# Optimization experiments

Hardware: AMD Instinct MI355X
Metric: run time of the kernel (lower is better)

## Reference

```python
import jax, jax.numpy as jnp
import numpy as np

DIM = 1024
NUM_HEADS = 1  # module's proj-after-squeeze only type-checks with 1 head
HEAD_DIM = DIM // NUM_HEADS
NQ = 8192
NK = 8192
B = 1


def setup_inputs() -> dict:
    key = jax.random.key(0)
    ks = jax.random.split(key, 12)
    s = 0.02  # weight init scale
    return {
        "q": jax.random.normal(ks[0], (NQ, B, DIM), jnp.float32),
        "k": jax.random.normal(ks[1], (NK, B, DIM), jnp.float32),
        "v": jax.random.normal(ks[2], (NK, B, DIM), jnp.float32),
        "ref_boxes": jax.random.uniform(ks[3], (NK, B, 4), jnp.float32),
        "query_boxes": jax.random.uniform(ks[4], (NQ, B, 4), jnp.float32),
        "Wq": jax.random.normal(ks[5], (DIM, DIM), jnp.float32) * s,
        "Wk": jax.random.normal(ks[6], (DIM, DIM), jnp.float32) * s,
        "Wv": jax.random.normal(ks[7], (DIM, DIM), jnp.float32) * s,
        "Wp": jax.random.normal(ks[8], (DIM, DIM), jnp.float32) * s,
        "bp": jnp.zeros((DIM,), jnp.float32),
        "W1": jax.random.normal(ks[9], (DIM, 2 * DIM), jnp.float32) * s,
        "b1": jnp.zeros((2 * DIM,), jnp.float32),
        "W2": jax.random.normal(ks[10], (2 * DIM, NUM_HEADS), jnp.float32) * s,
        "b2": jnp.zeros((NUM_HEADS,), jnp.float32),
    }


def _centers(boxes):  # [N, B, 4] -> [B, N, 2]
    c = (boxes[..., :2] + boxes[..., 2:]) * 0.5
    return jnp.transpose(c, (1, 0, 2))


def reference(q, k, v, ref_boxes, query_boxes, Wq, Wk, Wv, Wp, bp, W1, b1, W2, b2):
    Nq, Bsz, dim = q.shape
    Nk = k.shape[0]
    H = W2.shape[1]
    hd = dim // H
    scale = hd ** -0.5

    # bias_weight = sigmoid(MLP(var(k, dim=0)))  -- torch.var is unbiased (ddof=1)
    gfv = jnp.var(k, axis=0, ddof=1)                       # [B, dim]
    bias_weight = jax.nn.sigmoid(
        jax.nn.relu(gfv @ W1 + b1) @ W2 + b2
    )                                                       # [B, H]

    # seq-first -> batch-first, project, split heads
    qb = jnp.transpose(q, (1, 0, 2))                        # [B, Nq, dim]
    kb = jnp.transpose(k, (1, 0, 2))
    vb = jnp.transpose(v, (1, 0, 2))
    qh = (qb @ Wq).reshape(Bsz, Nq, H, hd).transpose(0, 2, 1, 3) * scale
    kh = (kb @ Wk).reshape(Bsz, Nk, H, hd).transpose(0, 2, 1, 3)
    vh = (vb @ Wv).reshape(Bsz, Nk, H, hd).transpose(0, 2, 1, 3)

    attn = jnp.einsum('bhqd,bhkd->bhqk', qh, kh)            # [B, H, Nq, Nk]

    # relative-position bias: per-head learned weight * (-pairwise box-center distance)
    cq = _centers(query_boxes)                              # [B, Nq, 2]
    cr = _centers(ref_boxes)                                # [B, Nk, 2]
    d2 = jnp.sum((cq[:, :, None, :] - cr[:, None, :, :]) ** 2, axis=-1)
    dist = jnp.sqrt(d2 + 1e-8)                              # [B, Nq, Nk]
    attn = attn - bias_weight[:, :, None, None] * dist[:, None, :, :]

    attn = jax.nn.softmax(attn, axis=-1)
    x = jnp.einsum('bhqk,bhkd->bhqd', attn, vh)             # [B, H, Nq, hd]
    x = jnp.squeeze(x)                                      # [Nq, dim] since B=H=1
    return x @ Wp + bp
```

## Files before the change

kernel.cpp:

```cpp
#include <hip/hip_runtime.h>
#include <math.h>

#define DIM 1024
#define NQ 8192
#define NK 8192

typedef unsigned short u16;
typedef __attribute__((ext_vector_type(8))) short short8;
typedef __attribute__((ext_vector_type(8))) u16 u16x8;
typedef __attribute__((ext_vector_type(4))) u16 u16x4;
typedef __attribute__((ext_vector_type(4))) float f32x4;
typedef __attribute__((address_space(1))) const unsigned int gu32;
typedef __attribute__((address_space(3))) unsigned int lu32;

__device__ inline u16 f2bf(float f) {
  unsigned u = __builtin_bit_cast(unsigned, f);
  u += 0x7fff + ((u >> 16) & 1);
  return (u16)(u >> 16);
}
__device__ inline float bf2f(u16 h) {
  unsigned u = ((unsigned)h) << 16;
  return __builtin_bit_cast(float, u);
}


__global__ void var_partial_kernel(const float* __restrict__ k,
                                   float* __restrict__ ps, float* __restrict__ pq) {
  int col = blockIdx.x * 256 + threadIdx.x;
  int r0  = blockIdx.y * 256;
  float s = 0.f, q = 0.f;
  for (int r = 0; r < 256; ++r) {
    float x = k[(size_t)(r0 + r) * DIM + col];
    s += x; q += x * x;
  }
  ps[blockIdx.y * DIM + col] = s;
  pq[blockIdx.y * DIM + col] = q;
}

__global__ void gfv_kernel(const float* __restrict__ ps, const float* __restrict__ pq,
                           float* __restrict__ gfv) {
  int col = blockIdx.x * 256 + threadIdx.x;
  float s = 0.f, q = 0.f;
  for (int c = 0; c < 32; ++c) { s += ps[c * DIM + col]; q += pq[c * DIM + col]; }
  const float n = 8192.f;
  gfv[col] = (q - s * s / n) / (n - 1.f);
}

__global__ void h1_partial_kernel(const float* __restrict__ gfv, const float* __restrict__ W1,
                                  float* __restrict__ h1p) {
  int j  = blockIdx.x * 256 + threadIdx.x;
  int d0 = blockIdx.y * 128;
  float acc = 0.f;
  for (int d = 0; d < 128; ++d)
    acc += gfv[d0 + d] * W1[(size_t)(d0 + d) * 2048 + j];
  h1p[blockIdx.y * 2048 + j] = acc;
}

__global__ void bw_kernel(const float* __restrict__ h1p, const float* __restrict__ b1,
                          const float* __restrict__ W2, const float* __restrict__ b2,
                          float* __restrict__ bw) {
  __shared__ float red[256];
  int t = threadIdx.x;
  float acc = 0.f;
  for (int i = 0; i < 8; ++i) {
    int j = i * 256 + t;
    float h = b1[j];
    for (int c = 0; c < 8; ++c) h += h1p[c * 2048 + j];
    h = fmaxf(h, 0.f);
    acc += h * W2[j];
  }
  red[t] = acc; __syncthreads();
  for (int s = 128; s > 0; s >>= 1) { if (t < s) red[t] += red[t + s]; __syncthreads(); }
  if (t == 0) bw[0] = 1.f / (1.f + __expf(-(red[0] + b2[0])));
}

__global__ void centers_kernel(const float4* __restrict__ qb, const float4* __restrict__ rb,
                               const float* __restrict__ bwp,
                               float2* __restrict__ cq, float2* __restrict__ cr,
                               float2* __restrict__ cqs, float2* __restrict__ crs) {
  int i = blockIdx.x * 256 + threadIdx.x;
  const float sc = bwp[0] * 1.44269504f;
  float4 a = qb[i];
  float2 c1 = make_float2(0.5f * (a.x + a.z), 0.5f * (a.y + a.w));
  cq[i] = c1;
  cqs[i] = make_float2(c1.x * sc, c1.y * sc);
  float4 b = rb[i];
  float2 c2 = make_float2(0.5f * (b.x + b.z), 0.5f * (b.y + b.w));
  cr[i] = c2;
  crs[i] = make_float2(c2.x * sc, c2.y * sc);
}


__global__ void f2bf3_kernel(const float4* __restrict__ a, const float4* __restrict__ b,
                             const float4* __restrict__ c, u16x4* __restrict__ oa,
                             u16x4* __restrict__ ob, u16x4* __restrict__ oc, int n4) {
  const float4* in = (blockIdx.y == 0) ? a : (blockIdx.y == 1) ? b : c;
  u16x4* out = (blockIdx.y == 0) ? oa : (blockIdx.y == 1) ? ob : oc;
  for (int i = blockIdx.x * 256 + threadIdx.x; i < n4; i += gridDim.x * 256) {
    float4 v = in[i];
    u16x4 o;
    o[0] = f2bf(v.x); o[1] = f2bf(v.y); o[2] = f2bf(v.z); o[3] = f2bf(v.w);
    out[i] = o;
  }
}

__global__ __launch_bounds__(256) void wtrans4_kernel(
    const float* __restrict__ W0, const float* __restrict__ W1,
    const float* __restrict__ W2, const float* __restrict__ W3,
    u16* __restrict__ T0, u16* __restrict__ T1, u16* __restrict__ T2, u16* __restrict__ T3) {
  const float* W = (blockIdx.z == 0) ? W0 : (blockIdx.z == 1) ? W1 : (blockIdx.z == 2) ? W2 : W3;
  u16* WT = (blockIdx.z == 0) ? T0 : (blockIdx.z == 1) ? T1 : (blockIdx.z == 2) ? T2 : T3;
  __shared__ float tile[64][65];
  const int t = threadIdx.x;
  const int kb = blockIdx.x * 64, nb = blockIdx.y * 64;
#pragma unroll
  for (int i = 0; i < 16; ++i) {
    int r = i * 4 + (t >> 6), c = t & 63;
    tile[c][r] = W[(size_t)(kb + r) * 1024 + nb + c];
  }
  __syncthreads();
#pragma unroll
  for (int i = 0; i < 16; ++i) {
    int n = i * 4 + (t >> 6), kk = t & 63;
    WT[(size_t)(nb + n) * 1024 + kb + kk] = f2bf(tile[n][kk]);
  }
}


#define TM 128
#define TN 128
#define TK 32

template <int OUT>
__global__ __launch_bounds__(256) void bgemm_kernel(
    const u16* __restrict__ A, const u16* __restrict__ Bt, void* __restrict__ C,
    const float* __restrict__ bias, int M, int N, int K, int ldc, float alpha) {
  __shared__ __align__(16) u16 As[TM * TK];
  __shared__ __align__(16) u16 Bs[TN * TK];

  const int t = threadIdx.x;
  const int l = t & 63;
  const int w = t >> 6;
  const int wm = w >> 1, wn = w & 1;
  const size_t row0 = (size_t)blockIdx.y * TM;
  const size_t col0 = (size_t)blockIdx.x * TN;

  f32x4 acc[4][4];
#pragma unroll
  for (int m = 0; m < 4; ++m)
#pragma unroll
    for (int n = 0; n < 4; ++n) acc[m][n] = (f32x4){0.f, 0.f, 0.f, 0.f};

  const int lane_r = l & 15;
  const int kgrp = (l >> 4) * 8;

  for (int k0 = 0; k0 < K; k0 += TK) {
#pragma unroll
    for (int j = 0; j < 2; ++j) {
      int idx = j * 256 + t;
      int r = idx >> 2, c8 = (idx & 3) << 3;
      __builtin_amdgcn_global_load_lds((gu32*)(A + (row0 + r) * K + k0 + c8),
                                       (lu32*)(As + idx * 8), 16, 0, 0);
      __builtin_amdgcn_global_load_lds((gu32*)(Bt + (col0 + r) * K + k0 + c8),
                                       (lu32*)(Bs + idx * 8), 16, 0, 0);
    }
    __syncthreads();

    short8 a[4], b[4];
#pragma unroll
    for (int m = 0; m < 4; ++m)
      a[m] = *(const short8*)&As[(wm * 64 + m * 16 + lane_r) * TK + kgrp];
#pragma unroll
    for (int n = 0; n < 4; ++n)
      b[n] = *(const short8*)&Bs[(wn * 64 + n * 16 + lane_r) * TK + kgrp];
#pragma unroll
    for (int m = 0; m < 4; ++m)
#pragma unroll
      for (int n = 0; n < 4; ++n)
        acc[m][n] = __builtin_amdgcn_mfma_f32_16x16x32_bf16(a[m], b[n], acc[m][n], 0, 0, 0);
    __syncthreads();
  }

#pragma unroll
  for (int m = 0; m < 4; ++m) {
#pragma unroll
    for (int n = 0; n < 4; ++n) {
      size_t col = col0 + wn * 64 + n * 16 + lane_r;
      size_t rbase = row0 + wm * 64 + m * 16 + (l >> 4) * 4;
      if (OUT == 0) {
        float bv = bias[col];
#pragma unroll
        for (int j = 0; j < 4; ++j)
          ((float*)C)[(rbase + j) * (size_t)ldc + col] = acc[m][n][j] * alpha + bv;
      } else if (OUT == 1) {
#pragma unroll
        for (int j = 0; j < 4; ++j)
          ((u16*)C)[(rbase + j) * (size_t)ldc + col] = f2bf(acc[m][n][j] * alpha);
      } else {
        u16x4 p;
#pragma unroll
        for (int j = 0; j < 4; ++j) p[j] = f2bf(acc[m][n][j] * alpha);
        *(u16x4*)&((u16*)C)[col * (size_t)ldc + rbase] = p;
      }
    }
  }
}


template <int VM>
__device__ __forceinline__ void waitvm() {
  if constexpr (VM == 4) asm volatile("s_waitcnt vmcnt(4)" ::: "memory");
  else asm volatile("s_waitcnt vmcnt(0)" ::: "memory");
}
#define FENCE asm volatile("" ::: "memory")
#define BARRIER do { FENCE; __builtin_amdgcn_s_barrier(); FENCE; } while (0)

#define SGA(UNIT, KT, BUF)                                                          \
  __builtin_amdgcn_global_load_lds(                                                 \
      (gu32*)(Agp + (size_t)((UNIT) * 64) * ldaB + (size_t)(KT) * 128),             \
      (lu32*)(smem + (BUF) * 16384 + (UNIT) * 4096 + tid * 8), 16, 0, 0)

#define SGB(UNIT, KT, BUF)                                                          \
  do {                                                                              \
    int _rp = (UNIT) * 64 + rr;                                                     \
    size_t _row = (size_t)(bn0 + ((_rp >> 5) & 3) * 64 + (_rp >> 7) * 32 + (_rp & 31)); \
    __builtin_amdgcn_global_load_lds(                                               \
        (gu32*)(Bgp + _row * ldbB + (size_t)(KT) * 128),                            \
        (lu32*)(smem + 32768 + (BUF) * 16384 + (UNIT) * 4096 + tid * 8), 16, 0, 0); \
  } while (0)

#define RDA4(DST, BO, MQ, KO)                                                       \
  _Pragma("unroll") for (int fr = 0; fr < 4; ++fr)                                  \
    DST[fr] = *(const short8*)(smemc + (BO) + aRd + (MQ) * 8192 + fr * 2048 + (KO));

#define RDB2(NQ_, KK, BO, KO)                                                       \
  _Pragma("unroll") for (int fc = 0; fc < 2; ++fc)                                  \
    bf[NQ_][KK][fc] = *(const short8*)(smemc + 65536 + (BO) + bRd + (NQ_) * 16384 + fc * 2048 + (KO));

#define MM8(AF, MQ, NQ_, KK)                                                        \
  do {                                                                              \
    __builtin_amdgcn_s_setprio(1);                                                  \
    _Pragma("unroll") for (int fr = 0; fr < 4; ++fr)                                \
    _Pragma("unroll") for (int fc = 0; fc < 2; ++fc)                                \
      acc[(MQ) * 4 + fr][(NQ_) * 2 + fc] = __builtin_amdgcn_mfma_f32_16x16x32_bf16( \
          AF[fr], bf[NQ_][KK][fc], acc[(MQ) * 4 + fr][(NQ_) * 2 + fc], 0, 0, 0);    \
    __builtin_amdgcn_s_setprio(0);                                                  \
  } while (0)

template <int OUT>
__global__ __launch_bounds__(512, 2) void gemm256_kernel(
    const u16* __restrict__ A, const u16* __restrict__ Bt, void* __restrict__ C,
    const float* __restrict__ bias, const float2* __restrict__ cqp,
    const float2* __restrict__ crp, const float* __restrict__ bwp,
    float* __restrict__ psum, int NT, int nTn, int tmb,
    size_t ldaB, size_t ldbB, int ldc, size_t kspanB, size_t cstride, float alpha) {
  __shared__ __align__(16) u16 smem[65536];
  const char* smemc = (const char*)smem;

  const int tid = threadIdx.x;
  const int l = tid & 63;
  const int wid = tid >> 6;
  const int wm = wid >> 2, wn = wid & 3;
  const int lane_r = l & 15;
  const int kq = l >> 4;
  const int rr = tid >> 3;

  const int bid = blockIdx.x;
  const int xcd = bid & 7;
  const int c = bid >> 3;
  const int tm = xcd * tmb + (c % tmb);
  const int tn = c / tmb;
  const int am0 = tm * 256, bn0 = tn * 256;
  const size_t kglob = kspanB * blockIdx.y;

  int band = 0;
  if (OUT == 2) { band = am0 >> 13; Bt += (size_t)band << 20; }

  const int kx = (lane_r & 7) << 4;
  const int koff0 = (kq << 4) ^ kx;
  const int koff1 = (64 | (kq << 4)) ^ kx;
  const int aRd = (wm * 128 + lane_r) * 128;
  const int bRd = (wn * 32 + lane_r) * 128;

  const int scol = ((tid & 7) ^ ((tid >> 3) & 7)) << 4;
  const char* Agp = (const char*)A + (size_t)(am0 + rr) * ldaB + kglob + scol;
  const char* Bgp = (const char*)Bt + kglob + scol;

  f32x4 acc[8][4];
#pragma unroll
  for (int i = 0; i < 8; ++i)
#pragma unroll
    for (int j = 0; j < 4; ++j) acc[i][j] = (f32x4){0.f, 0.f, 0.f, 0.f};

  short8 afP[4], afQ[4], bf[2][2][2];

  SGA(0, 0, 0); SGA(2, 0, 0); SGB(0, 0, 0); SGB(1, 0, 0);
  SGB(2, 0, 0); SGB(3, 0, 0); SGA(1, 0, 0); SGA(3, 0, 0);
  waitvm<0>();
  BARRIER;
  RDA4(afP, 0, 0, koff0);
  RDB2(0, 0, 0, koff0);

  for (int t = 0; t < NT; ++t) {
    const int bo = (t & 1) * 32768;
    const int nbo = bo ^ 32768;
    const int nb = (t & 1) ^ 1;
    const bool more = (t + 1 < NT);
    if (more) { SGA(0, t + 1, nb); SGA(2, t + 1, nb); }
    RDB2(1, 0, bo, koff0);
    MM8(afP, 0, 0, 0);
    if (more) { SGB(0, t + 1, nb); SGB(1, t + 1, nb); }
    RDA4(afQ, bo, 1, koff0);
    MM8(afP, 0, 1, 0);
    if (more) { SGB(2, t + 1, nb); SGB(3, t + 1, nb); }
    RDB2(0, 1, bo, koff1);
    MM8(afQ, 1, 1, 0);
    if (more) { SGA(1, t + 1, nb); SGA(3, t + 1, nb); }
    RDA4(afP, bo, 1, koff1);
    MM8(afQ, 1, 0, 0);
    RDB2(1, 1, bo, koff1);
    MM8(afP, 1, 0, 1);
    RDA4(afQ, bo, 0, koff1);
    MM8(afP, 1, 1, 1);
    MM8(afQ, 0, 1, 1);
    waitvm<4>();
    BARRIER;
    if (more) { RDA4(afP, nbo, 0, koff0); RDB2(0, 0, nbo, koff0); }
    MM8(afQ, 0, 0, 1);
    waitvm<0>();
    BARRIER;
  }

  if (OUT == 4) {
    const float sc = bwp[0] * 1.44269504f;
    const float eps2 = sc * sc * 1e-8f;
    float* psld = (float*)smem;
    float2 crv[4];
#pragma unroll
    for (int fc2 = 0; fc2 < 4; ++fc2) crv[fc2] = crp[bn0 + wn * 64 + fc2 * 16 + lane_r];
#pragma unroll
    for (int fp = 0; fp < 8; ++fp) {
      float rs[4] = {0.f, 0.f, 0.f, 0.f};
      int rbase = am0 + wm * 128 + fp * 16 + kq * 4;
#pragma unroll
      for (int j = 0; j < 4; ++j) {
        float2 cqv = cqp[rbase + j];
#pragma unroll
        for (int fc2 = 0; fc2 < 4; ++fc2) {
          float dx = cqv.x - crv[fc2].x, dy = cqv.y - crv[fc2].y;
          float d2v = fmaf(dx, dx, fmaf(dy, dy, eps2));
          float D;
          asm("v_sqrt_f32 %0, %1" : "=v"(D) : "v"(d2v));
          float l2 = fmaf(acc[fp][fc2][j], 1.44269504f, -D);
          float pv;
          asm("v_exp_f32 %0, %1" : "=v"(pv) : "v"(l2));
          rs[j] += pv;
          int col = bn0 + wn * 64 + fc2 * 16 + lane_r;
          ((u16*)C)[(size_t)(rbase + j) * ldc + col] = f2bf(pv);
        }
      }
#pragma unroll
      for (int j = 0; j < 4; ++j) {
        float s = rs[j];
        s += __shfl_xor(s, 1); s += __shfl_xor(s, 2);
        s += __shfl_xor(s, 4); s += __shfl_xor(s, 8);
        if (lane_r == 0)
          psld[(wm * 128 + fp * 16 + kq * 4 + j) * 4 + wn] = s;
      }
    }
    __syncthreads();
    if (tid < 256) {
      float s = psld[tid * 4] + psld[tid * 4 + 1] + psld[tid * 4 + 2] + psld[tid * 4 + 3];
      psum[(size_t)tn * NQ + am0 + tid] = s;
    }
    return;
  }
#pragma unroll
  for (int fp = 0; fp < 8; ++fp) {
#pragma unroll
    for (int fc2 = 0; fc2 < 4; ++fc2) {
      int row = am0 + wm * 128 + fp * 16 + kq * 4;
      int col = bn0 + wn * 64 + fc2 * 16 + lane_r;
      if (OUT == 0) {
#pragma unroll
        for (int j = 0; j < 4; ++j)
          ((u16*)C)[(size_t)(row + j) * ldc + col] = f2bf(acc[fp][fc2][j] * alpha);
      } else if (OUT == 1) {
        u16* Cp = (u16*)C + cstride * blockIdx.y;
#pragma unroll
        for (int j = 0; j < 4; ++j)
          Cp[(size_t)(row + j) * ldc + col] = f2bf(acc[fp][fc2][j]);
      } else if (OUT == 3) {
        float* Cf = (float*)C;
        float bv = bias[col];
#pragma unroll
        for (int j = 0; j < 4; ++j)
          Cf[(size_t)(row + j) * ldc + col] = acc[fp][fc2][j] * alpha + bv;
      } else {
        int arow = row & 8191;
        if (band < 2) {
          u16* D = (u16*)C + ((size_t)band << 23);
          float a2 = (band == 0) ? 0.03125f : 1.f;
#pragma unroll
          for (int j = 0; j < 4; ++j)
            D[(size_t)(arow + j) * DIM + col] = f2bf(acc[fp][fc2][j] * a2);
        } else {
          u16* D = (u16*)C + ((size_t)2 << 23);
          u16x4 pk;
#pragma unroll
          for (int j = 0; j < 4; ++j) pk[j] = f2bf(acc[fp][fc2][j]);
          *(u16x4*)&D[(size_t)col * NK + arow] = pk;
        }
      }
    }
  }
}


__global__ void rowinv_kernel(const float* __restrict__ psum, float* __restrict__ inv) {
  int r = blockIdx.x * 256 + threadIdx.x;
  float s = 0.f;
#pragma unroll
  for (int t = 0; t < 32; ++t) s += psum[(size_t)t * NQ + r];
  inv[r] = 1.f / s;
}


__global__ void combine4_kernel(const u16x8* __restrict__ p, const float* __restrict__ inv,
                                u16x8* __restrict__ out) {
  const size_t st = (size_t)NQ * DIM / 8;
  size_t i = (size_t)blockIdx.x * 256 + threadIdx.x;
  u16x8 a = p[i], b = p[i + st], c = p[i + 2 * st], d = p[i + 3 * st];
  float iv = inv[i >> 7];
  u16x8 o;
#pragma unroll
  for (int j = 0; j < 8; ++j)
    o[j] = f2bf((bf2f(a[j]) + bf2f(b[j]) + bf2f(c[j]) + bf2f(d[j])) * iv);
  out[i] = o;
}


__global__ __launch_bounds__(256) void softmax_bias_bf16_kernel(
    u16* __restrict__ S, const float2* __restrict__ cq, const float2* __restrict__ cr,
    const float* __restrict__ bwp, int qr0) {
  __shared__ float red[256];
  const int t = threadIdx.x;
  u16* row = S + (size_t)blockIdx.x * NK;
  const float2 cqv = cq[qr0 + blockIdx.x];
  const float bw = bwp[0];

  float l[32];
  float mx = -1e30f;
#pragma unroll
  for (int i = 0; i < 4; ++i) {
    int base = (i * 256 + t) * 8;
    u16x8 u = *(const u16x8*)&row[base];
#pragma unroll
    for (int j = 0; j < 8; ++j) {
      float x = bf2f(u[j]);
      float2 c = cr[base + j];
      float dx = cqv.x - c.x, dy = cqv.y - c.y;
      float lv = x - bw * sqrtf(dx * dx + dy * dy + 1e-8f);
      l[i * 8 + j] = lv;
      mx = fmaxf(mx, lv);
    }
  }
  red[t] = mx; __syncthreads();
  for (int s = 128; s > 0; s >>= 1) { if (t < s) red[t] = fmaxf(red[t], red[t + s]); __syncthreads(); }
  mx = red[0]; __syncthreads();

  float sum = 0.f;
#pragma unroll
  for (int i = 0; i < 32; ++i) { float e = __expf(l[i] - mx); l[i] = e; sum += e; }
  red[t] = sum; __syncthreads();
  for (int s = 128; s > 0; s >>= 1) { if (t < s) red[t] += red[t + s]; __syncthreads(); }
  float inv = 1.f / red[0];

#pragma unroll
  for (int i = 0; i < 4; ++i) {
    int base = (i * 256 + t) * 8;
    u16x8 o;
#pragma unroll
    for (int j = 0; j < 8; ++j) o[j] = f2bf(l[i * 8 + j] * inv);
    *(u16x8*)&row[base] = o;
  }
}


extern "C" void kernel_launch(void* const* d_in, const int* in_sizes, int n_in,
                              void* d_out, int out_size, void* d_ws, size_t ws_size,
                              hipStream_t stream) {
  const float* q  = (const float*)d_in[0];
  const float* k  = (const float*)d_in[1];
  const float* v  = (const float*)d_in[2];
  const float* rb = (const float*)d_in[3];
  const float* qb = (const float*)d_in[4];
  const float* Wq = (const float*)d_in[5];
  const float* Wk = (const float*)d_in[6];
  const float* Wv = (const float*)d_in[7];
  const float* Wp = (const float*)d_in[8];
  const float* bp = (const float*)d_in[9];
  const float* W1 = (const float*)d_in[10];
  const float* b1 = (const float*)d_in[11];
  const float* W2 = (const float*)d_in[12];
  const float* b2 = (const float*)d_in[13];
  float* out = (float*)d_out;

  char* p = (char*)d_ws;
  const size_t PROJB = (size_t)NQ * DIM * sizeof(u16);
  u16* qbf = (u16*)p;            p += PROJB;
  u16* kbf = (u16*)p;            p += PROJB;
  u16* vbf = (u16*)p;            p += PROJB;
  u16* qh  = (u16*)p;            p += PROJB;
  u16* kh  = (u16*)p;            p += PROJB;
  u16* vhT = (u16*)p;            p += PROJB;
  u16* WqT = (u16*)p;            p += (size_t)DIM * DIM * 2;
  u16* WkT = (u16*)p;            p += (size_t)DIM * DIM * 2;
  u16* WvT = (u16*)p;            p += (size_t)DIM * DIM * 2;
  u16* WpT = (u16*)p;            p += (size_t)DIM * DIM * 2;
  float* cq  = (float*)p;        p += 2 * NQ * 4;
  float* cr  = (float*)p;        p += 2 * NK * 4;
  float* cqs = (float*)p;        p += 2 * NQ * 4;
  float* crs = (float*)p;        p += 2 * NK * 4;
  float* ps  = (float*)p;        p += 32 * DIM * 4;
  float* pq  = (float*)p;        p += 32 * DIM * 4;
  float* gfv = (float*)p;        p += DIM * 4;
  float* h1p = (float*)p;        p += 8 * 2048 * 4;
  float* bw  = (float*)p;        p += 64;
  float* psum = (float*)p;       p += (size_t)32 * NQ * 4;
  float* rinv = (float*)p;       p += (size_t)NQ * 4;
  size_t fixed_b = (size_t)(p - (char*)d_ws);

  int SR = 256;
  for (int cand = 8192; cand >= 256; cand >>= 1) {
    if (fixed_b + (size_t)cand * (NK + DIM) * 2 <= ws_size) { SR = cand; break; }
  }
  u16* Sbuf = (u16*)p;
  u16* Obuf = Sbuf + (size_t)SR * NK;

  var_partial_kernel<<<dim3(4, 32), 256, 0, stream>>>(k, ps, pq);
  gfv_kernel<<<4, 256, 0, stream>>>(ps, pq, gfv);
  h1_partial_kernel<<<dim3(8, 8), 256, 0, stream>>>(gfv, W1, h1p);
  bw_kernel<<<1, 256, 0, stream>>>(h1p, b1, W2, b2, bw);
  centers_kernel<<<32, 256, 0, stream>>>((const float4*)qb, (const float4*)rb, bw,
                                         (float2*)cq, (float2*)cr,
                                         (float2*)cqs, (float2*)crs);

  const int N4 = NQ * DIM / 4;
  f2bf3_kernel<<<dim3(1024, 3), 256, 0, stream>>>(
      (const float4*)q, (const float4*)k, (const float4*)v,
      (u16x4*)qbf, (u16x4*)kbf, (u16x4*)vbf, N4);
  wtrans4_kernel<<<dim3(16, 16, 4), 256, 0, stream>>>(Wq, Wk, Wv, Wp, WqT, WkT, WvT, WpT);

  gemm256_kernel<2><<<dim3(384, 1), 512, 0, stream>>>(
      qbf, WqT, qh, nullptr, nullptr, nullptr, nullptr, nullptr,
      16, 4, 12, 2048, 2048, DIM, 0, 0, 1.f);

  if (SR == 8192) {
    gemm256_kernel<4><<<dim3(1024, 1), 512, 0, stream>>>(
        qh, kh, Sbuf, nullptr, (const float2*)cqs, (const float2*)crs, bw, psum,
        16, 32, 4, 2048, 2048, NK, 0, 0, 1.f);
    rowinv_kernel<<<32, 256, 0, stream>>>(psum, rinv);
    gemm256_kernel<1><<<dim3(128, 4), 512, 0, stream>>>(
        Sbuf, vhT, qbf, nullptr, nullptr, nullptr, nullptr, nullptr,
        32, 4, 4, 16384, 16384, DIM, 4096, (size_t)NQ * DIM, 1.f);
    combine4_kernel<<<4096, 256, 0, stream>>>((const u16x8*)qbf, rinv, (u16x8*)Obuf);
    gemm256_kernel<3><<<dim3(128, 1), 512, 0, stream>>>(
        Obuf, WpT, out, bp, nullptr, nullptr, nullptr, nullptr,
        16, 4, 4, 2048, 2048, DIM, 0, 0, 1.f);
  } else {
    for (int s0 = 0; s0 < NQ; s0 += SR) {
      bgemm_kernel<1><<<dim3(NK / TN, SR / TM), 256, 0, stream>>>(
          qh + (size_t)s0 * DIM, kh, Sbuf, nullptr, SR, NK, DIM, NK, 1.f);
      softmax_bias_bf16_kernel<<<SR, 256, 0, stream>>>(
          Sbuf, (const float2*)cq, (const float2*)cr, bw, s0);
      bgemm_kernel<1><<<dim3(DIM / TN, SR / TM), 256, 0, stream>>>(
          Sbuf, vhT, Obuf, nullptr, SR, DIM, NK, DIM, 1.f);
      bgemm_kernel<0><<<dim3(DIM / TN, SR / TM), 256, 0, stream>>>(
          Obuf, WpT, out + (size_t)s0 * DIM, bp, SR, DIM, DIM, DIM, 1.f);
    }
  }
}
```

Before: 436.8 us.

## Add 8-phase pipelined GEMM kernel for PV and output projection

Adds a new gemm8p kernel used for the attention-times-V GEMM and the final projection. It keeps a two-tile-ahead global-to-LDS prefetch with vmcnt(6) waits, and splits each K-tile into four MFMA phases separated by barriers, each phase using both k-halves. The goal is to hide global load latency better than the previous one-tile-ahead schedule. In exchange it issues more barriers per tile, which can serialize waves and offset the gain.

```diff
diff --git a/kernel.cpp b/kernel.cpp
--- a/kernel.cpp
+++ b/kernel.cpp
@@ -209,7 +209,8 @@
 
 template <int VM>
 __device__ __forceinline__ void waitvm() {
-  if constexpr (VM == 4) asm volatile("s_waitcnt vmcnt(4)" ::: "memory");
+  if constexpr (VM == 6) asm volatile("s_waitcnt vmcnt(6)" ::: "memory");
+  else if constexpr (VM == 4) asm volatile("s_waitcnt vmcnt(4)" ::: "memory");
   else asm volatile("s_waitcnt vmcnt(0)" ::: "memory");
 }
 #define FENCE asm volatile("" ::: "memory")
@@ -247,6 +248,49 @@
     __builtin_amdgcn_s_setprio(0);                                                  \
   } while (0)
 
+#define MM16Q(MQ, NQ_)                                                              \
+  do {                                                                              \
+    __builtin_amdgcn_s_setprio(1);                                                  \
+    _Pragma("unroll") for (int fr = 0; fr < 4; ++fr)                                \
+    _Pragma("unroll") for (int fc = 0; fc < 2; ++fc) {                              \
+      acc[(MQ) * 4 + fr][(NQ_) * 2 + fc] = __builtin_amdgcn_mfma_f32_16x16x32_bf16( \
+          aqk0[fr], bf[NQ_][0][fc], acc[(MQ) * 4 + fr][(NQ_) * 2 + fc], 0, 0, 0);   \
+      acc[(MQ) * 4 + fr][(NQ_) * 2 + fc] = __builtin_amdgcn_mfma_f32_16x16x32_bf16( \
+          aqk1[fr], bf[NQ_][1][fc], acc[(MQ) * 4 + fr][(NQ_) * 2 + fc], 0, 0, 0);   \
+    }                                                                               \
+    __builtin_amdgcn_s_setprio(0);                                                  \
+  } while (0)
+
+#define GEMM_SETUP                                                                  \
+  __shared__ __align__(16) u16 smem[65536];                                         \
+  const char* smemc = (const char*)smem;                                            \
+  const int tid = threadIdx.x;                                                      \
+  const int l = tid & 63;                                                           \
+  const int wid = tid >> 6;                                                         \
+  const int wm = wid >> 2, wn = wid & 3;                                            \
+  const int lane_r = l & 15;                                                        \
+  const int kq = l >> 4;                                                            \
+  const int rr = tid >> 3;                                                          \
+  const int bid = blockIdx.x;                                                       \
+  const int xcd = bid & 7;                                                          \
+  const int c = bid >> 3;                                                           \
+  const int tm = xcd * tmb + (c % tmb);                                             \
+  const int tn = c / tmb;                                                           \
+  const int am0 = tm * 256, bn0 = tn * 256;                                         \
+  const size_t kglob = kspanB * blockIdx.y;                                         \
+  const int kx = (lane_r & 7) << 4;                                                 \
+  const int koff0 = (kq << 4) ^ kx;                                                 \
+  const int koff1 = (64 | (kq << 4)) ^ kx;                                          \
+  const int aRd = (wm * 128 + lane_r) * 128;                                        \
+  const int bRd = (wn * 32 + lane_r) * 128;                                         \
+  const int scol = ((tid & 7) ^ ((tid >> 3) & 7)) << 4;                             \
+  const char* Agp = (const char*)A + (size_t)(am0 + rr) * ldaB + kglob + scol;      \
+  const char* Bgp = (const char*)Bt + kglob + scol;                                 \
+  f32x4 acc[8][4];                                                                  \
+  _Pragma("unroll") for (int i = 0; i < 8; ++i)                                     \
+  _Pragma("unroll") for (int j = 0; j < 4; ++j) acc[i][j] = (f32x4){0.f, 0.f, 0.f, 0.f};
+
+
 template <int OUT>
 __global__ __launch_bounds__(512, 2) void gemm256_kernel(
     const u16* __restrict__ A, const u16* __restrict__ Bt, void* __restrict__ C,
@@ -254,43 +298,13 @@
     const float2* __restrict__ crp, const float* __restrict__ bwp,
     float* __restrict__ psum, int NT, int nTn, int tmb,
     size_t ldaB, size_t ldbB, int ldc, size_t kspanB, size_t cstride, float alpha) {
-  __shared__ __align__(16) u16 smem[65536];
-  const char* smemc = (const char*)smem;
-
-  const int tid = threadIdx.x;
-  const int l = tid & 63;
-  const int wid = tid >> 6;
-  const int wm = wid >> 2, wn = wid & 3;
-  const int lane_r = l & 15;
-  const int kq = l >> 4;
-  const int rr = tid >> 3;
-
-  const int bid = blockIdx.x;
-  const int xcd = bid & 7;
-  const int c = bid >> 3;
-  const int tm = xcd * tmb + (c % tmb);
-  const int tn = c / tmb;
-  const int am0 = tm * 256, bn0 = tn * 256;
-  const size_t kglob = kspanB * blockIdx.y;
+  GEMM_SETUP;
 
   int band = 0;
-  if (OUT == 2) { band = am0 >> 13; Bt += (size_t)band << 20; }
-
-  const int kx = (lane_r & 7) << 4;
-  const int koff0 = (kq << 4) ^ kx;
-  const int koff1 = (64 | (kq << 4)) ^ kx;
-  const int aRd = (wm * 128 + lane_r) * 128;
-  const int bRd = (wn * 32 + lane_r) * 128;
-
-  const int scol = ((tid & 7) ^ ((tid >> 3) & 7)) << 4;
-  const char* Agp = (const char*)A + (size_t)(am0 + rr) * ldaB + kglob + scol;
-  const char* Bgp = (const char*)Bt + kglob + scol;
-
-  f32x4 acc[8][4];
-#pragma unroll
-  for (int i = 0; i < 8; ++i)
-#pragma unroll
-    for (int j = 0; j < 4; ++j) acc[i][j] = (f32x4){0.f, 0.f, 0.f, 0.f};
+  const u16* Bt2 = Bt;
+  if (OUT == 2) { band = am0 >> 13; Bt2 = Bt + ((size_t)band << 20); }
+  const char* Bgp2 = (const char*)Bt2 + kglob + scol;
+  #define Bgp Bgp2
 
   short8 afP[4], afQ[4], bf[2][2][2];
 
@@ -330,6 +344,7 @@
     waitvm<0>();
     BARRIER;
   }
+  #undef Bgp
 
   if (OUT == 4) {
     const float sc = bwp[0] * 1.44269504f;
@@ -385,17 +400,6 @@
 #pragma unroll
         for (int j = 0; j < 4; ++j)
           ((u16*)C)[(size_t)(row + j) * ldc + col] = f2bf(acc[fp][fc2][j] * alpha);
-      } else if (OUT == 1) {
-        u16* Cp = (u16*)C + cstride * blockIdx.y;
-#pragma unroll
-        for (int j = 0; j < 4; ++j)
-          Cp[(size_t)(row + j) * ldc + col] = f2bf(acc[fp][fc2][j]);
-      } else if (OUT == 3) {
-        float* Cf = (float*)C;
-        float bv = bias[col];
-#pragma unroll
-        for (int j = 0; j < 4; ++j)
-          Cf[(size_t)(row + j) * ldc + col] = acc[fp][fc2][j] * alpha + bv;
       } else {
         int arow = row & 8191;
         if (band < 2) {
@@ -411,6 +415,75 @@
           for (int j = 0; j < 4; ++j) pk[j] = f2bf(acc[fp][fc2][j]);
           *(u16x4*)&D[(size_t)col * NK + arow] = pk;
         }
+      }
+    }
+  }
+}
+
+
+template <int OUT>
+__global__ __launch_bounds__(512, 2) void gemm8p_kernel(
+    const u16* __restrict__ A, const u16* __restrict__ Bt, void* __restrict__ C,
+    const float* __restrict__ bias, int NT, int nTn, int tmb,
+    size_t ldaB, size_t ldbB, int ldc, size_t kspanB, size_t cstride, float alpha) {
+  GEMM_SETUP;
+
+  short8 aqk0[4], aqk1[4], bf[2][2][2];
+
+  SGA(0, 0, 0); SGA(2, 0, 0); SGB(0, 0, 0); SGB(1, 0, 0);
+  SGB(2, 0, 0); SGB(3, 0, 0); SGA(1, 0, 0); SGA(3, 0, 0);
+  if (NT > 1) {
+    SGA(0, 1, 1); SGA(2, 1, 1);
+    SGB(2, 1, 1); SGB(3, 1, 1);
+    SGA(1, 1, 1); SGA(3, 1, 1);
+  }
+  waitvm<6>();
+  BARRIER;
+
+  for (int t = 0; t < NT; ++t) {
+    const int bo = (t & 1) * 32768;
+    const int cb = t & 1, nb = cb ^ 1;
+    const bool m1 = (t + 1 < NT), m2 = (t + 2 < NT);
+    RDA4(aqk0, bo, 0, koff0); RDA4(aqk1, bo, 0, koff1);
+    RDB2(0, 0, bo, koff0); RDB2(0, 1, bo, koff1);
+    if (m1) { SGB(0, t + 1, nb); SGB(1, t + 1, nb); }
+    BARRIER;
+    MM16Q(0, 0);
+    BARRIER;
+    RDB2(1, 0, bo, koff0); RDB2(1, 1, bo, koff1);
+    if (m2) { SGA(0, t + 2, cb); SGA(2, t + 2, cb); }
+    BARRIER;
+    MM16Q(0, 1);
+    BARRIER;
+    RDA4(aqk0, bo, 1, koff0); RDA4(aqk1, bo, 1, koff1);
+    if (m2) { SGB(2, t + 2, cb); SGB(3, t + 2, cb); }
+    BARRIER;
+    MM16Q(1, 1);
+    BARRIER;
+    if (m2) { SGA(1, t + 2, cb); SGA(3, t + 2, cb); }
+    BARRIER;
+    MM16Q(1, 0);
+    if (m2) waitvm<6>(); else waitvm<0>();
+    BARRIER;
+  }
+
+#pragma unroll
+  for (int fp = 0; fp < 8; ++fp) {
+#pragma unroll
+    for (int fc2 = 0; fc2 < 4; ++fc2) {
+      int row = am0 + wm * 128 + fp * 16 + kq * 4;
+      int col = bn0 + wn * 64 + fc2 * 16 + lane_r;
+      if (OUT == 1) {
+        u16* Cp = (u16*)C + cstride * blockIdx.y;
+#pragma unroll
+        for (int j = 0; j < 4; ++j)
+          Cp[(size_t)(row + j) * ldc + col] = f2bf(acc[fp][fc2][j]);
+      } else {
+        float* Cf = (float*)C;
+        float bv = bias[col];
+#pragma unroll
+        for (int j = 0; j < 4; ++j)
+          Cf[(size_t)(row + j) * ldc + col] = acc[fp][fc2][j] * alpha + bv;
       }
     }
   }
@@ -561,13 +634,12 @@
         qh, kh, Sbuf, nullptr, (const float2*)cqs, (const float2*)crs, bw, psum,
         16, 32, 4, 2048, 2048, NK, 0, 0, 1.f);
     rowinv_kernel<<<32, 256, 0, stream>>>(psum, rinv);
-    gemm256_kernel<1><<<dim3(128, 4), 512, 0, stream>>>(
-        Sbuf, vhT, qbf, nullptr, nullptr, nullptr, nullptr, nullptr,
-        32, 4, 4, 16384, 16384, DIM, 4096, (size_t)NQ * DIM, 1.f);
+    gemm8p_kernel<1><<<dim3(128, 4), 512, 0, stream>>>(
+        Sbuf, vhT, qbf, nullptr, 32, 4, 4, 16384, 16384, DIM, 4096,
+        (size_t)NQ * DIM, 1.f);
     combine4_kernel<<<4096, 256, 0, stream>>>((const u16x8*)qbf, rinv, (u16x8*)Obuf);
-    gemm256_kernel<3><<<dim3(128, 1), 512, 0, stream>>>(
-        Obuf, WpT, out, bp, nullptr, nullptr, nullptr, nullptr,
-        16, 4, 4, 2048, 2048, DIM, 0, 0, 1.f);
+    gemm8p_kernel<3><<<dim3(128, 1), 512, 0, stream>>>(
+        Obuf, WpT, out, bp, 16, 4, 4, 2048, 2048, DIM, 0, 0, 1.f);
   } else {
     for (int s0 = 0; s0 < NQ; s0 += SR) {
       bgemm_kernel<1><<<dim3(NK / TN, SR / TM), 256, 0, stream>>>(
```

New measurement: 443.4 us. No clear change (+1.5%).
